# Kernel tuning notes

Measured on AMD Instinct MI355X. Metric: run time of the kernel, lower is better.

## Reference

```python
import jax, jax.numpy as jnp
import numpy as np

N, E, T, IN, H, OUT = 100000, 800000, 8, 3, 32, 64


def _lstm_dir(pre, Whh, bhh, reverse):
    # pre: [T, E, 4H] precomputed input contribution (x @ W_ih^T + b_ih)
    Hh = Whh.shape[1]

    def step(carry, xt):
        h, c = carry
        g = xt + h @ Whh.T + bhh  # [E, 4H], pytorch gate order i,f,g,o
        i = jax.nn.sigmoid(g[:, :Hh])
        f = jax.nn.sigmoid(g[:, Hh:2 * Hh])
        gg = jnp.tanh(g[:, 2 * Hh:3 * Hh])
        o = jax.nn.sigmoid(g[:, 3 * Hh:])
        c = f * c + i * gg
        h = o * jnp.tanh(c)
        return (h, c), None

    init = (jnp.zeros((pre.shape[1], Hh), pre.dtype),
            jnp.zeros((pre.shape[1], Hh), pre.dtype))
    (h, c), _ = jax.lax.scan(step, init, pre, reverse=reverse)
    return c  # final cell state [E, H]


def _mlp(x, W1, W2):
    # MLP(num_layers=2, bias=False): lin1 -> relu -> lin2
    return jax.nn.relu(x @ W1.T) @ W2.T


def setup_inputs() -> dict:
    key = jax.random.key(0)
    ks = jax.random.split(key, 18)
    s = 0.1
    inp = {
        "x": jax.random.normal(ks[0], (N, IN), jnp.float32),
        "edge_traj": jax.random.normal(ks[1], (E, T, 6), jnp.float32),
        "w_ih_f": jax.random.normal(ks[2], (4 * H, 6), jnp.float32) * s,
        "w_hh_f": jax.random.normal(ks[3], (4 * H, H), jnp.float32) * s,
        "b_ih_f": jax.random.normal(ks[4], (4 * H,), jnp.float32) * s,
        "b_hh_f": jax.random.normal(ks[5], (4 * H,), jnp.float32) * s,
        "w_ih_b": jax.random.normal(ks[6], (4 * H, 6), jnp.float32) * s,
        "w_hh_b": jax.random.normal(ks[7], (4 * H, H), jnp.float32) * s,
        "b_ih_b": jax.random.normal(ks[8], (4 * H,), jnp.float32) * s,
        "b_hh_b": jax.random.normal(ks[9], (4 * H,), jnp.float32) * s,
        "coor_w1": jax.random.normal(ks[10], (H, IN), jnp.float32) * s,
        "coor_w2": jax.random.normal(ks[11], (H, H), jnp.float32) * s,
        "nn2_w1": jax.random.normal(ks[12], (H, 3 * H), jnp.float32) * s,
        "nn2_w2": jax.random.normal(ks[13], (H, H), jnp.float32) * s,
        "nn_w1": jax.random.normal(ks[14], (H, H), jnp.float32) * s,
        "nn_w2": jax.random.normal(ks[15], (OUT, H), jnp.float32) * s,
        "edge_index": jax.random.randint(ks[16], (2, E), 0, N, dtype=jnp.int32),
    }
    return inp


def reference(x, edge_traj, w_ih_f, w_hh_f, b_ih_f, b_hh_f,
              w_ih_b, w_hh_b, b_ih_b, b_hh_b,
              coor_w1, coor_w2, nn2_w1, nn2_w2, nn_w1, nn_w2, edge_index):
    # bidirectional 1-layer LSTM over edge trajectories; edge attr = c_t.mean(dim=0)
    pre_f = jnp.einsum('etf,gf->teg', edge_traj, w_ih_f) + b_ih_f
    pre_b = jnp.einsum('etf,gf->teg', edge_traj, w_ih_b) + b_ih_b
    c_f = _lstm_dir(pre_f, w_hh_f, b_hh_f, reverse=False)
    c_b = _lstm_dir(pre_b, w_hh_b, b_hh_b, reverse=True)
    traj_encoding = 0.5 * (c_f + c_b)  # [E, H]

    coor = _mlp(x, coor_w1, coor_w2)  # [N, H]

    src, dst = edge_index[0], edge_index[1]  # flow: source_to_target
    # message: nn2(cat[x_i, x_j, edge_attr]) per edge
    msg_in = jnp.concatenate([coor[dst], coor[src], traj_encoding], axis=-1)  # [E, 3H]
    msg = _mlp(msg_in, nn2_w1, nn2_w2)  # [E, H]
    agg = jax.ops.segment_sum(msg, dst, num_segments=N)  # [N, H]

    out = _mlp(agg, nn_w1, nn_w2)  # [N, OUT]; (note: GINEConv.forward skips (1+eps)*x)
    return out.sum(axis=0)  # [OUT]
```

## Files before the change

### kernel.cpp

```cpp
#include <hip/hip_runtime.h>
#include <hip/hip_bf16.h>

typedef __attribute__((ext_vector_type(8))) short    bf16x8;
typedef __attribute__((ext_vector_type(4))) float    f32x4;
typedef __attribute__((ext_vector_type(4))) unsigned u32x4;

#define MTPW 4
#define LOG2E  1.442695041f
#define LOG2E2 2.885390082f
#define MFMA __builtin_amdgcn_mfma_f32_16x16x32_bf16

__device__ __forceinline__ float rcp_(float v){ return __builtin_amdgcn_rcpf(v); }
__device__ __forceinline__ float exp2_(float v){ return __builtin_amdgcn_exp2f(v); }
__device__ __forceinline__ unsigned pk2(float lo, float hi){
    __hip_bfloat162 h = __float22bfloat162_rn(float2{lo, hi});
    return *(unsigned*)&h;
}
__device__ __forceinline__ float lo2f(unsigned u){ return __uint_as_float(u << 16); }
__device__ __forceinline__ float hi2f(unsigned u){ return __uint_as_float(u & 0xFFFF0000u); }

union U4 { bf16x8 v; unsigned u[4]; };

__device__ __forceinline__ bf16x8 ldw8(const float* __restrict__ p){
    const float4 a = *(const float4*)p;
    const float4 b = *(const float4*)(p + 4);
    U4 r;
    r.u[0] = pk2(a.x, a.y); r.u[1] = pk2(a.z, a.w);
    r.u[2] = pk2(b.x, b.y); r.u[3] = pk2(b.z, b.w);
    return r.v;
}
__device__ __forceinline__ bf16x8 ldw8p(const float* __restrict__ rowp, int lq, float s){
    const float4 a = *(const float4*)(rowp + 4*lq);
    const float4 b = *(const float4*)(rowp + 16 + 4*lq);
    U4 r;
    r.u[0] = pk2(a.x*s, a.y*s); r.u[1] = pk2(a.z*s, a.w*s);
    r.u[2] = pk2(b.x*s, b.y*s); r.u[3] = pk2(b.z*s, b.w*s);
    return r.v;
}

#define LDS_RD8(d0,d1,d2,d3,d4,d5,d6,d7,O0,O1,O2,O3,O4,O5,O6,O7)            \
  asm volatile("ds_read_b128 %0, %8 offset:" O0 "\n\t"                      \
               "ds_read_b128 %1, %8 offset:" O1 "\n\t"                      \
               "ds_read_b128 %2, %8 offset:" O2 "\n\t"                      \
               "ds_read_b128 %3, %8 offset:" O3 "\n\t"                      \
               "ds_read_b128 %4, %8 offset:" O4 "\n\t"                      \
               "ds_read_b128 %5, %8 offset:" O5 "\n\t"                      \
               "ds_read_b128 %6, %8 offset:" O6 "\n\t"                      \
               "ds_read_b128 %7, %8 offset:" O7 "\n\t"                      \
               "s_waitcnt lgkmcnt(0)"                                       \
               : "=&v"(d0),"=&v"(d1),"=&v"(d2),"=&v"(d3),                   \
                 "=&v"(d4),"=&v"(d5),"=&v"(d6),"=&v"(d7)                    \
               : "v"(lds_addr))

__device__ __forceinline__ bf16x8 bc8(u32x4 x){ return __builtin_bit_cast(bf16x8, x); }

__device__ __forceinline__ void gates4_first(const f32x4 ai, const f32x4 ag, const f32x4 ao,
                                             float c[4], float h[4]){
#pragma unroll
    for (int r = 0; r < 4; ++r) {
        const float Ea = exp2_(ai[r]);
        const float Eg = exp2_(ag[r]);
        const float Eo = exp2_(ao[r]);
        c[r] = (Eg - 1.f) * rcp_((Ea + 1.f) * (Eg + 1.f));
        const float Ec = exp2_(LOG2E2 * c[r]);
        h[r] = (Ec - 1.f) * rcp_((Eo + 1.f) * (Ec + 1.f));
    }
}
__device__ __forceinline__ void gates4_mid(const f32x4 ai, const f32x4 af,
                                           const f32x4 ag, const f32x4 ao,
                                           float c[4], float h[4]){
#pragma unroll
    for (int r = 0; r < 4; ++r) {
        const float Ea = exp2_(ai[r]);
        const float Ef = exp2_(af[r]);
        const float Eg = exp2_(ag[r]);
        const float Eo = exp2_(ao[r]);
        const float p  = (Ea + 1.f) * (Eg + 1.f);
        const float f1 = Ef + 1.f;
        const float num = fmaf(c[r], p, (Eg - 1.f) * f1);
        c[r] = num * rcp_(p * f1);
        const float Ec = exp2_(LOG2E2 * c[r]);
        h[r] = (Ec - 1.f) * rcp_((Eo + 1.f) * (Ec + 1.f));
    }
}
__device__ __forceinline__ void gates4_last(const f32x4 ai, const f32x4 af,
                                            const f32x4 ag, float c[4]){
#pragma unroll
    for (int r = 0; r < 4; ++r) {
        const float Ea = exp2_(ai[r]);
        const float Ef = exp2_(af[r]);
        const float Eg = exp2_(ag[r]);
        const float p  = (Ea + 1.f) * (Eg + 1.f);
        const float f1 = Ef + 1.f;
        const float num = fmaf(c[r], p, (Eg - 1.f) * f1);
        c[r] = num * rcp_(p * f1);
    }
}

__global__ __launch_bounds__(256) void coor_kernel(
    const float* __restrict__ x, const float* __restrict__ w1,
    const float* __restrict__ w2, unsigned short* __restrict__ coorb, int N)
{
    __shared__ float sW1[96];
    __shared__ float sW2[1024];
    const int tid = threadIdx.x;
    if (tid < 96) sW1[tid] = w1[tid];
    for (int i = tid; i < 1024; i += 256) sW2[i] = w2[i];
    __syncthreads();
    int n = blockIdx.x * 256 + tid;
    if (n >= N) return;
    const float x0 = x[n*3+0], x1 = x[n*3+1], x2 = x[n*3+2];
    float h[32];
#pragma unroll
    for (int k = 0; k < 32; ++k)
        h[k] = fmaxf(sW1[k*3+0]*x0 + sW1[k*3+1]*x1 + sW1[k*3+2]*x2, 0.0f);
    union { uint4 q[4]; unsigned u[16]; } st;
#pragma unroll
    for (int p = 0; p < 16; ++p) {
        float a0 = 0.f, a1 = 0.f;
#pragma unroll
        for (int k = 0; k < 32; ++k) {
            a0 += sW2[(2*p)  *32 + k] * h[k];
            a1 += sW2[(2*p+1)*32 + k] * h[k];
        }
        st.u[p] = pk2(a0, a1);
    }
    uint4* cp = (uint4*)(coorb + (size_t)n * 32);
#pragma unroll
    for (int w = 0; w < 4; ++w) cp[w] = st.q[w];
}

template<int DIR>
__global__ __launch_bounds__(256, 4) void lstm_kernel(
    const float* __restrict__ edge_traj,
    const float* __restrict__ w_ih, const float* __restrict__ w_hh,
    const float* __restrict__ b_ih, const float* __restrict__ b_hh,
    unsigned* __restrict__ cbuf, int E)
{
    __shared__ unsigned lds_w[4096];
    const int tid = threadIdx.x;
    for (int i = tid; i < 512; i += 256) {
        const int m = i >> 6, ln = i & 63;
        const int le2 = ln & 15, lq2 = ln >> 4;
        const int row = 16*m + le2;
        const float s = (m == 4 || m == 5) ? LOG2E2 : -LOG2E;
        const float4 a = *(const float4*)(w_hh + row*32 + 4*lq2);
        const float4 b = *(const float4*)(w_hh + row*32 + 16 + 4*lq2);
        unsigned* wp = &lds_w[(size_t)i * 4];
        wp[0] = pk2(a.x*s, a.y*s); wp[1] = pk2(a.z*s, a.w*s);
        wp[2] = pk2(b.x*s, b.y*s); wp[3] = pk2(b.z*s, b.w*s);
        unsigned* xp = &lds_w[(size_t)(512 + i) * 4];
        if (lq2 == 0) {
            const float* p = w_ih + row * 6;
            xp[0] = pk2(p[0]*s, p[1]*s);
            xp[1] = pk2(p[2]*s, p[3]*s);
            xp[2] = pk2(p[4]*s, p[5]*s);
            xp[3] = pk2((b_ih[row] + b_hh[row])*s, 0.f);
        } else {
            xp[0] = 0u; xp[1] = 0u; xp[2] = 0u; xp[3] = 0u;
        }
    }
    __syncthreads();

    const int lane = tid & 63;
    const int wid  = tid >> 6;
    const int le   = lane & 15;
    const int lq   = lane >> 4;
    const bool l0  = (lq == 0);
    const unsigned lds_addr = (unsigned)(size_t)lds_w + (unsigned)lane * 16u;
    const f32x4 Z4 = {0.f, 0.f, 0.f, 0.f};

    const long tile = (long)blockIdx.x * 4 + wid;
    const long e0 = tile * 16;
    if (e0 >= E) return;
    const long er = e0 + le;
    const bool valid = er < E;
    const float* xb = edge_traj + (valid ? er : (E - 1)) * 48;

    U4 hf; hf.u[0]=hf.u[1]=hf.u[2]=hf.u[3]=0u;
    float cl[4]={0,0,0,0}, ch[4]={0,0,0,0};

#pragma unroll
    for (int t = 0; t < 8; ++t) {
        const int te = DIR ? (7 - t) : t;
        U4 xf;
        {
            const float* xp = xb + te * 6;
            const float2 a  = *(const float2*)xp;
            const float2 b2 = *(const float2*)(xp + 2);
            const float2 c2 = *(const float2*)(xp + 4);
            xf.u[0] = l0 ? pk2(a.x, a.y)   : 0u;
            xf.u[1] = l0 ? pk2(b2.x, b2.y) : 0u;
            xf.u[2] = l0 ? pk2(c2.x, c2.y) : 0u;
            xf.u[3] = l0 ? 0x3f80u         : 0u;
        }

        u32x4 f0,f1,f2,f3,f4,f5,f6,f7;
        LDS_RD8(f0,f1,f2,f3,f4,f5,f6,f7,
                "0","2048","4096","6144","8192","10240","12288","14336");
        f32x4 ai = MFMA(bc8(f4), xf.v, Z4, 0,0,0);
        f32x4 af = Z4, ao = Z4;
        if (t != 0) af = MFMA(bc8(f5), xf.v, Z4, 0,0,0);
        f32x4 ag = MFMA(bc8(f6), xf.v, Z4, 0,0,0);
        if (t != 7) ao = MFMA(bc8(f7), xf.v, Z4, 0,0,0);
        if (t > 0) {
            ai = MFMA(bc8(f0), hf.v, ai, 0,0,0);
            af = MFMA(bc8(f1), hf.v, af, 0,0,0);
            ag = MFMA(bc8(f2), hf.v, ag, 0,0,0);
            if (t != 7) ao = MFMA(bc8(f3), hf.v, ao, 0,0,0);
        }
        u32x4 g0,g1,g2,g3,g4,g5,g6,g7;
        LDS_RD8(g0,g1,g2,g3,g4,g5,g6,g7,
                "1024","3072","5120","7168","9216","11264","13312","15360");

        float hl[4], hh[4];
        if (t == 0)      gates4_first(ai, ag, ao, cl, hl);
        else if (t == 7) gates4_last(ai, af, ag, cl);
        else             gates4_mid(ai, af, ag, ao, cl, hl);

        f32x4 bi = MFMA(bc8(g4), xf.v, Z4, 0,0,0);
        f32x4 bf = Z4, bo = Z4;
        if (t != 0) bf = MFMA(bc8(g5), xf.v, Z4, 0,0,0);
        f32x4 bg = MFMA(bc8(g6), xf.v, Z4, 0,0,0);
        if (t != 7) bo = MFMA(bc8(g7), xf.v, Z4, 0,0,0);
        if (t > 0) {
            bi = MFMA(bc8(g0), hf.v, bi, 0,0,0);
            bf = MFMA(bc8(g1), hf.v, bf, 0,0,0);
            bg = MFMA(bc8(g2), hf.v, bg, 0,0,0);
            if (t != 7) bo = MFMA(bc8(g3), hf.v, bo, 0,0,0);
        }
        if (t == 0)      gates4_first(bi, bg, bo, ch, hh);
        else if (t == 7) gates4_last(bi, bf, bg, ch);
        else             gates4_mid(bi, bf, bg, bo, ch, hh);

        if (t < 7) {
            hf.u[0] = pk2(hl[0], hl[1]); hf.u[1] = pk2(hl[2], hl[3]);
            hf.u[2] = pk2(hh[0], hh[1]); hf.u[3] = pk2(hh[2], hh[3]);
        }
    }

    if (valid) {
        U4 cw;
        cw.u[0] = pk2(cl[0], cl[1]);
        cw.u[1] = pk2(cl[2], cl[3]);
        cw.u[2] = pk2(ch[0], ch[1]);
        cw.u[3] = pk2(ch[2], ch[3]);
        unsigned* dp = cbuf + er * 16 + lq * 4;
        if (DIR == 0) {
            *(uint4*)dp = *(uint4*)cw.u;
        } else {
            const uint4 f = *(const uint4*)dp;
            uint4 o;
            o.x = pk2(0.5f*(lo2f(f.x)+lo2f(cw.u[0])), 0.5f*(hi2f(f.x)+hi2f(cw.u[0])));
            o.y = pk2(0.5f*(lo2f(f.y)+lo2f(cw.u[1])), 0.5f*(hi2f(f.y)+hi2f(cw.u[1])));
            o.z = pk2(0.5f*(lo2f(f.z)+lo2f(cw.u[2])), 0.5f*(hi2f(f.z)+hi2f(cw.u[2])));
            o.w = pk2(0.5f*(lo2f(f.w)+lo2f(cw.u[3])), 0.5f*(hi2f(f.w)+hi2f(cw.u[3])));
            *(uint4*)dp = o;
        }
    }
}

__global__ __launch_bounds__(256, 4) void msg_kernel(
    unsigned* trmsg,
    const float* __restrict__ nn2_w1, const float* __restrict__ nn2_w2,
    const int* __restrict__ edge_index,
    const unsigned short* __restrict__ coorb, int E)
{
    const int lane = threadIdx.x & 63;
    const int wid  = threadIdx.x >> 6;
    const int le   = lane & 15;
    const int lq   = lane >> 4;
    const f32x4 Z4 = {0.f, 0.f, 0.f, 0.f};

    bf16x8 w1a[2][3], w2a[2];
#pragma unroll
    for (int mm = 0; mm < 2; ++mm) {
        const int row = 16*mm + le;
        w1a[mm][0] = ldw8(nn2_w1 + row*96 +  8*lq);
        w1a[mm][1] = ldw8(nn2_w1 + row*96 + 32 + 8*lq);
        w1a[mm][2] = ldw8p(nn2_w1 + row*96 + 64, lq, 1.0f);
        w2a[mm]    = ldw8p(nn2_w2 + row*32, lq, 1.0f);
    }

    const long gw = (long)blockIdx.x * 4 + wid;
    for (int it = 0; it < MTPW; ++it) {
        const long tile = gw * MTPW + it;
        const long e0 = tile * 16;
        if (e0 >= E) break;
        const long e_raw = e0 + le;
        const bool valid = e_raw < E;
        const long ec = valid ? e_raw : (E - 1);

        U4 tf;
        if (valid) *(uint4*)tf.u = *(const uint4*)(trmsg + e_raw * 16 + lq * 4);
        else tf.u[0] = tf.u[1] = tf.u[2] = tf.u[3] = 0u;

        const int src = edge_index[ec];
        const int dst = edge_index[E + ec];
        U4 df, sf;
        {
            const uint4 dv = *(const uint4*)(coorb + (size_t)dst*32 + lq*8);
            const uint4 sv = *(const uint4*)(coorb + (size_t)src*32 + lq*8);
            df.u[0]=dv.x; df.u[1]=dv.y; df.u[2]=dv.z; df.u[3]=dv.w;
            sf.u[0]=sv.x; sf.u[1]=sv.y; sf.u[2]=sv.z; sf.u[3]=sv.w;
        }

        f32x4 h1[2];
#pragma unroll
        for (int mm = 0; mm < 2; ++mm) {
            f32x4 a = MFMA(w1a[mm][0], df.v, Z4, 0,0,0);
            a = MFMA(w1a[mm][1], sf.v, a, 0,0,0);
            a = MFMA(w1a[mm][2], tf.v, a, 0,0,0);
            h1[mm] = a;
        }
        U4 gf;
        gf.u[0] = pk2(fmaxf(h1[0][0],0.f), fmaxf(h1[0][1],0.f));
        gf.u[1] = pk2(fmaxf(h1[0][2],0.f), fmaxf(h1[0][3],0.f));
        gf.u[2] = pk2(fmaxf(h1[1][0],0.f), fmaxf(h1[1][1],0.f));
        gf.u[3] = pk2(fmaxf(h1[1][2],0.f), fmaxf(h1[1][3],0.f));

        const f32x4 o0 = MFMA(w2a[0], gf.v, Z4, 0,0,0);
        const f32x4 o1 = MFMA(w2a[1], gf.v, Z4, 0,0,0);
        if (valid) {
            U4 cw;
            cw.u[0] = pk2(o0[0], o0[1]);
            cw.u[1] = pk2(o0[2], o0[3]);
            cw.u[2] = pk2(o1[0], o1[1]);
            cw.u[3] = pk2(o1[2], o1[3]);
            *(uint4*)(trmsg + e_raw * 16 + lq * 4) = *(uint4*)cw.u;
        }
    }
}

__global__ __launch_bounds__(256) void hist_kernel(
    const int* __restrict__ ei, int* __restrict__ cnt, int E)
{
    const int e = blockIdx.x*256 + threadIdx.x;
    if (e < E) atomicAdd(&cnt[ei[E + e]], 1);
}

__global__ __launch_bounds__(256) void scan1_kernel(
    const int* __restrict__ cnt, int* __restrict__ bsum, int N)
{
    __shared__ int sp[4];
    const int tid = threadIdx.x;
    const int n = blockIdx.x*256 + tid;
    int c = (n < N) ? cnt[n] : 0;
#pragma unroll
    for (int m = 1; m < 64; m <<= 1) c += __shfl_xor(c, m, 64);
    if ((tid & 63) == 0) sp[tid >> 6] = c;
    __syncthreads();
    if (tid == 0) bsum[blockIdx.x] = sp[0] + sp[1] + sp[2] + sp[3];
}

__global__ __launch_bounds__(512) void scan2_kernel(
    int* __restrict__ bsum, int* __restrict__ offs, int nblk, int E, int N)
{
    __shared__ int s[512];
    const int tid = threadIdx.x;
    const int v = (tid < nblk) ? bsum[tid] : 0;
    s[tid] = v;
    __syncthreads();
    for (int off = 1; off < 512; off <<= 1) {
        const int t = (tid >= off) ? s[tid - off] : 0;
        __syncthreads();
        s[tid] += t;
        __syncthreads();
    }
    if (tid < nblk) bsum[tid] = s[tid] - v;
    if (tid == 0) offs[N] = E;
}

__global__ __launch_bounds__(256) void scan3_kernel(
    const int* __restrict__ cnt, const int* __restrict__ bsum,
    int* __restrict__ offs, int* __restrict__ cursor, int N)
{
    __shared__ int s[256];
    const int tid = threadIdx.x;
    const int n = blockIdx.x*256 + tid;
    const int v = (n < N) ? cnt[n] : 0;
    s[tid] = v;
    __syncthreads();
    for (int off = 1; off < 256; off <<= 1) {
        const int t = (tid >= off) ? s[tid - off] : 0;
        __syncthreads();
        s[tid] += t;
        __syncthreads();
    }
    if (n < N) {
        const int o = bsum[blockIdx.x] + s[tid] - v;
        offs[n] = o;
        cursor[n] = o;
    }
}

__global__ __launch_bounds__(256) void fill_kernel(
    const int* __restrict__ ei, int* __restrict__ cursor,
    int* __restrict__ eidx, int E)
{
    const int e = blockIdx.x*256 + threadIdx.x;
    if (e < E) {
        const int p = atomicAdd(&cursor[ei[E + e]], 1);
        eidx[p] = e;
    }
}

__global__ __launch_bounds__(256) void gather_kernel(
    const unsigned* __restrict__ msg, const int* __restrict__ offs,
    const int* __restrict__ eidx, float* __restrict__ aggv, int N)
{
    const int lane = threadIdx.x & 63;
    const int wid  = threadIdx.x >> 6;
    const int g  = lane >> 4;
    const int le = lane & 15;
    const int n = blockIdx.x*16 + wid*4 + g;
    if (n >= N) return;
    const int beg = offs[n], end = offs[n+1];
    float sx = 0.f, sy = 0.f;
    for (int i = beg; i < end; ++i) {
        const unsigned w = msg[(size_t)eidx[i]*16 + le];
        sx += lo2f(w); sy += hi2f(w);
    }
    *(float2*)(aggv + (size_t)n*32 + 2*le) = float2{sx, sy};
}

__global__ __launch_bounds__(256) void agg_kernel(
    const float* __restrict__ aggv, const float* __restrict__ nn_w1,
    float* __restrict__ partials, int N)
{
    __shared__ float sW[1024];
    __shared__ float sP[4][32];
    const int tid = threadIdx.x;
    for (int i = tid; i < 1024; i += 256) {
        const int jj = i >> 5, s = i & 31, q = s >> 3, j = s & 7;
        const int col = (j < 4) ? (4*q + j) : (16 + 4*q + (j - 4));
        sW[i] = nn_w1[jj*32 + col];
    }
    __syncthreads();
    const int n = blockIdx.x*256 + tid;
    float h[32];
    if (n < N) {
        float a[32];
        const float4* ap = (const float4*)(aggv + (size_t)n*32);
#pragma unroll
        for (int k4 = 0; k4 < 8; ++k4) {
            const float4 v = ap[k4];
            a[k4*4]=v.x; a[k4*4+1]=v.y; a[k4*4+2]=v.z; a[k4*4+3]=v.w;
        }
#pragma unroll
        for (int jj = 0; jj < 32; ++jj) {
            float acc = 0.f;
#pragma unroll
            for (int k = 0; k < 32; ++k) acc += sW[jj*32+k]*a[k];
            h[jj] = fmaxf(acc, 0.f);
        }
    } else {
#pragma unroll
        for (int jj = 0; jj < 32; ++jj) h[jj] = 0.f;
    }
#pragma unroll
    for (int m = 1; m < 64; m <<= 1) {
#pragma unroll
        for (int k = 0; k < 32; ++k) h[k] += __shfl_xor(h[k], m, 64);
    }
    if ((tid & 63) == 0) {
#pragma unroll
        for (int k = 0; k < 32; ++k) sP[tid >> 6][k] = h[k];
    }
    __syncthreads();
    if (tid < 32)
        partials[(size_t)blockIdx.x * 32 + tid]
            = sP[0][tid] + sP[1][tid] + sP[2][tid] + sP[3][tid];
}

__global__ __launch_bounds__(256) void reduce_kernel(
    const float* __restrict__ partials, const float* __restrict__ nn_w2,
    float* __restrict__ out, int nblk)
{
    __shared__ float sR[8][32];
    __shared__ float sS[32];
    const int tid = threadIdx.x;
    const int col = tid & 31;
    const int row = tid >> 5;
    float s = 0.f;
    for (int i = row; i < nblk; i += 8) s += partials[(size_t)i*32 + col];
    sR[row][col] = s;
    __syncthreads();
    if (row == 0) {
        float t = 0.f;
#pragma unroll
        for (int r = 0; r < 8; ++r) t += sR[r][col];
        sS[col] = t;
    }
    __syncthreads();
    if (tid < 64) {
        float acc = 0.f;
#pragma unroll
        for (int k = 0; k < 32; ++k) acc += nn_w2[tid*32+k] * sS[k];
        out[tid] = acc;
    }
}

extern "C" void kernel_launch(void* const* d_in, const int* in_sizes, int n_in,
                              void* d_out, int out_size, void* d_ws, size_t ws_size,
                              hipStream_t stream)
{
    const float* x         = (const float*)d_in[0];
    const float* edge_traj = (const float*)d_in[1];
    const float* w_ih_f    = (const float*)d_in[2];
    const float* w_hh_f    = (const float*)d_in[3];
    const float* b_ih_f    = (const float*)d_in[4];
    const float* b_hh_f    = (const float*)d_in[5];
    const float* w_ih_b    = (const float*)d_in[6];
    const float* w_hh_b    = (const float*)d_in[7];
    const float* b_ih_b    = (const float*)d_in[8];
    const float* b_hh_b    = (const float*)d_in[9];
    const float* coor_w1   = (const float*)d_in[10];
    const float* coor_w2   = (const float*)d_in[11];
    const float* nn2_w1    = (const float*)d_in[12];
    const float* nn2_w2    = (const float*)d_in[13];
    const float* nn_w1     = (const float*)d_in[14];
    const float* nn_w2     = (const float*)d_in[15];
    const int* edge_index  = (const int*)d_in[16];
    const int N = in_sizes[0] / 3;
    const int E = in_sizes[16] / 2;
    const int nblk = (N + 255) / 256;

    float* aggv = (float*)d_ws;
    float* partials = aggv + (size_t)N * 32;
    unsigned short* coorb = (unsigned short*)(partials + (size_t)nblk * 32);
    unsigned* cbuf = (unsigned*)(coorb + (size_t)N * 32);
    int* cnt    = (int*)(cbuf + (size_t)E * 16);
    int* offs   = cnt + N;
    int* cursor = offs + N + 1;
    int* eidx   = cursor + N;
    int* bsum   = eidx + E;

    (void)hipMemsetAsync(cnt, 0, (size_t)N * sizeof(int), stream);

    coor_kernel<<<nblk, 256, 0, stream>>>(x, coor_w1, coor_w2, coorb, N);

    const long tiles   = ((long)E + 15) / 16;
    const int  lblocks = (int)((tiles + 3) / 4);
    lstm_kernel<0><<<lblocks, 256, 0, stream>>>(edge_traj,
        w_ih_f, w_hh_f, b_ih_f, b_hh_f, cbuf, E);
    lstm_kernel<1><<<lblocks, 256, 0, stream>>>(edge_traj,
        w_ih_b, w_hh_b, b_ih_b, b_hh_b, cbuf, E);

    const int eblk = (E + 255) / 256;
    hist_kernel<<<eblk, 256, 0, stream>>>(edge_index, cnt, E);
    scan1_kernel<<<nblk, 256, 0, stream>>>(cnt, bsum, N);
    scan2_kernel<<<1, 512, 0, stream>>>(bsum, offs, nblk, E, N);
    scan3_kernel<<<nblk, 256, 0, stream>>>(cnt, bsum, offs, cursor, N);
    fill_kernel<<<eblk, 256, 0, stream>>>(edge_index, cursor, eidx, E);

    const int mblocks = (int)((tiles + 4*MTPW - 1) / (4*MTPW));
    msg_kernel<<<mblocks, 256, 0, stream>>>(cbuf, nn2_w1, nn2_w2,
        edge_index, coorb, E);

    gather_kernel<<<(N + 15)/16, 256, 0, stream>>>(cbuf, offs, eidx, aggv, N);
    agg_kernel<<<nblk, 256, 0, stream>>>(aggv, nn_w1, partials, N);
    reduce_kernel<<<1, 256, 0, stream>>>(partials, nn_w2, (float*)d_out, nblk);
}
```

Before: 607.0 us.

## Fuse forward and backward LSTM directions into one interleaved kernel

Merges the two per-direction LSTM launches into a single kernel that keeps both directions' weights in LDS and runs the forward and backward recurrences interleaved per timestep. This removes one launch, the second pass over edge_traj, and the read-modify-write of the cell buffer. Interleaving two independent dependency chains is meant to hide MFMA and transcendental latency. In exchange it doubles LDS use to 32 KB per block and raises register pressure, which could lower occupancy under the 4-block launch bound.

```diff
diff --git a/kernel.cpp b/kernel.cpp
--- a/kernel.cpp
+++ b/kernel.cpp
@@ -38,7 +38,7 @@
     return r.v;
 }
 
-#define LDS_RD8(d0,d1,d2,d3,d4,d5,d6,d7,O0,O1,O2,O3,O4,O5,O6,O7)            \
+#define LDS_RD8(AD,d0,d1,d2,d3,d4,d5,d6,d7,O0,O1,O2,O3,O4,O5,O6,O7)         \
   asm volatile("ds_read_b128 %0, %8 offset:" O0 "\n\t"                      \
                "ds_read_b128 %1, %8 offset:" O1 "\n\t"                      \
                "ds_read_b128 %2, %8 offset:" O2 "\n\t"                      \
@@ -50,9 +50,21 @@
                "s_waitcnt lgkmcnt(0)"                                       \
                : "=&v"(d0),"=&v"(d1),"=&v"(d2),"=&v"(d3),                   \
                  "=&v"(d4),"=&v"(d5),"=&v"(d6),"=&v"(d7)                    \
-               : "v"(lds_addr))
+               : "v"(AD))
 
 __device__ __forceinline__ bf16x8 bc8(u32x4 x){ return __builtin_bit_cast(bf16x8, x); }
+
+#define GRP(AI,AF,AG,AO, Q0,Q1,Q2,Q3,Q4,Q5,Q6,Q7, XF, HF)                   \
+    AI = MFMA(bc8(Q4), XF.v, Z4, 0,0,0);                                    \
+    AF = (t != 0) ? MFMA(bc8(Q5), XF.v, Z4, 0,0,0) : Z4;                    \
+    AG = MFMA(bc8(Q6), XF.v, Z4, 0,0,0);                                    \
+    AO = (t != 7) ? MFMA(bc8(Q7), XF.v, Z4, 0,0,0) : Z4;                    \
+    if (t > 0) {                                                            \
+        AI = MFMA(bc8(Q0), HF.v, AI, 0,0,0);                                \
+        AF = MFMA(bc8(Q1), HF.v, AF, 0,0,0);                                \
+        AG = MFMA(bc8(Q2), HF.v, AG, 0,0,0);                                \
+        if (t != 7) AO = MFMA(bc8(Q3), HF.v, AO, 0,0,0);                    \
+    }
 
 __device__ __forceinline__ void gates4_first(const f32x4 ai, const f32x4 ag, const f32x4 ao,
                                              float c[4], float h[4]){
@@ -96,6 +108,10 @@
         c[r] = num * rcp_(p * f1);
     }
 }
+#define GATES(AI,AF,AG,AO,C,H)                                              \
+    if (t == 0)      gates4_first(AI, AG, AO, C, H);                        \
+    else if (t == 7) gates4_last(AI, AF, AG, C);                            \
+    else             gates4_mid(AI, AF, AG, AO, C, H);
 
 __global__ __launch_bounds__(256) void coor_kernel(
     const float* __restrict__ x, const float* __restrict__ w1,
@@ -130,32 +146,39 @@
     for (int w = 0; w < 4; ++w) cp[w] = st.q[w];
 }
 
-template<int DIR>
 __global__ __launch_bounds__(256, 4) void lstm_kernel(
     const float* __restrict__ edge_traj,
-    const float* __restrict__ w_ih, const float* __restrict__ w_hh,
-    const float* __restrict__ b_ih, const float* __restrict__ b_hh,
+    const float* __restrict__ w_ih_f, const float* __restrict__ w_hh_f,
+    const float* __restrict__ b_ih_f, const float* __restrict__ b_hh_f,
+    const float* __restrict__ w_ih_b, const float* __restrict__ w_hh_b,
+    const float* __restrict__ b_ih_b, const float* __restrict__ b_hh_b,
     unsigned* __restrict__ cbuf, int E)
 {
-    __shared__ unsigned lds_w[4096];
-    const int tid = threadIdx.x;
-    for (int i = tid; i < 512; i += 256) {
-        const int m = i >> 6, ln = i & 63;
+    __shared__ unsigned lds_w[8192];
+    const int tid = threadIdx.x;
+    for (int i = tid; i < 1024; i += 256) {
+        const int dir = i >> 9;
+        const int idx = i & 511;
+        const int m = idx >> 6, ln = idx & 63;
         const int le2 = ln & 15, lq2 = ln >> 4;
         const int row = 16*m + le2;
         const float s = (m == 4 || m == 5) ? LOG2E2 : -LOG2E;
-        const float4 a = *(const float4*)(w_hh + row*32 + 4*lq2);
-        const float4 b = *(const float4*)(w_hh + row*32 + 16 + 4*lq2);
-        unsigned* wp = &lds_w[(size_t)i * 4];
+        const float* whh = dir ? w_hh_b : w_hh_f;
+        const float* wih = dir ? w_ih_b : w_ih_f;
+        const float* bi  = dir ? b_ih_b : b_ih_f;
+        const float* bh  = dir ? b_hh_b : b_hh_f;
+        const float4 a = *(const float4*)(whh + row*32 + 4*lq2);
+        const float4 b = *(const float4*)(whh + row*32 + 16 + 4*lq2);
+        unsigned* wp = &lds_w[(size_t)dir*4096 + (size_t)idx*4];
         wp[0] = pk2(a.x*s, a.y*s); wp[1] = pk2(a.z*s, a.w*s);
         wp[2] = pk2(b.x*s, b.y*s); wp[3] = pk2(b.z*s, b.w*s);
-        unsigned* xp = &lds_w[(size_t)(512 + i) * 4];
+        unsigned* xp = &lds_w[(size_t)dir*4096 + 2048 + (size_t)idx*4];
         if (lq2 == 0) {
-            const float* p = w_ih + row * 6;
+            const float* p = wih + row * 6;
             xp[0] = pk2(p[0]*s, p[1]*s);
             xp[1] = pk2(p[2]*s, p[3]*s);
             xp[2] = pk2(p[4]*s, p[5]*s);
-            xp[3] = pk2((b_ih[row] + b_hh[row])*s, 0.f);
+            xp[3] = pk2((bi[row] + bh[row])*s, 0.f);
         } else {
             xp[0] = 0u; xp[1] = 0u; xp[2] = 0u; xp[3] = 0u;
         }
@@ -167,7 +190,8 @@
     const int le   = lane & 15;
     const int lq   = lane >> 4;
     const bool l0  = (lq == 0);
-    const unsigned lds_addr = (unsigned)(size_t)lds_w + (unsigned)lane * 16u;
+    const unsigned adF = (unsigned)(size_t)lds_w + (unsigned)lane * 16u;
+    const unsigned adB = adF + 16384u;
     const f32x4 Z4 = {0.f, 0.f, 0.f, 0.f};
 
     const long tile = (long)blockIdx.x * 4 + wid;
@@ -177,86 +201,79 @@
     const bool valid = er < E;
     const float* xb = edge_traj + (valid ? er : (E - 1)) * 48;
 
-    U4 hf; hf.u[0]=hf.u[1]=hf.u[2]=hf.u[3]=0u;
-    float cl[4]={0,0,0,0}, ch[4]={0,0,0,0};
+    U4 hfF, hfB;
+    hfF.u[0]=hfF.u[1]=hfF.u[2]=hfF.u[3]=0u;
+    hfB.u[0]=hfB.u[1]=hfB.u[2]=hfB.u[3]=0u;
+    float clF[4]={0,0,0,0}, chF[4]={0,0,0,0};
+    float clB[4]={0,0,0,0}, chB[4]={0,0,0,0};
 
 #pragma unroll
     for (int t = 0; t < 8; ++t) {
-        const int te = DIR ? (7 - t) : t;
-        U4 xf;
+        U4 xfF, xfB;
         {
-            const float* xp = xb + te * 6;
+            const float* xp = xb + t * 6;
             const float2 a  = *(const float2*)xp;
             const float2 b2 = *(const float2*)(xp + 2);
             const float2 c2 = *(const float2*)(xp + 4);
-            xf.u[0] = l0 ? pk2(a.x, a.y)   : 0u;
-            xf.u[1] = l0 ? pk2(b2.x, b2.y) : 0u;
-            xf.u[2] = l0 ? pk2(c2.x, c2.y) : 0u;
-            xf.u[3] = l0 ? 0x3f80u         : 0u;
-        }
-
-        u32x4 f0,f1,f2,f3,f4,f5,f6,f7;
-        LDS_RD8(f0,f1,f2,f3,f4,f5,f6,f7,
+            xfF.u[0] = l0 ? pk2(a.x, a.y)   : 0u;
+            xfF.u[1] = l0 ? pk2(b2.x, b2.y) : 0u;
+            xfF.u[2] = l0 ? pk2(c2.x, c2.y) : 0u;
+            xfF.u[3] = l0 ? 0x3f80u         : 0u;
+        }
+        {
+            const float* xp = xb + (7 - t) * 6;
+            const float2 a  = *(const float2*)xp;
+            const float2 b2 = *(const float2*)(xp + 2);
+            const float2 c2 = *(const float2*)(xp + 4);
+            xfB.u[0] = l0 ? pk2(a.x, a.y)   : 0u;
+            xfB.u[1] = l0 ? pk2(b2.x, b2.y) : 0u;
+            xfB.u[2] = l0 ? pk2(c2.x, c2.y) : 0u;
+            xfB.u[3] = l0 ? 0x3f80u         : 0u;
+        }
+
+        u32x4 a0,a1,a2,a3,a4,a5,a6,a7;
+        LDS_RD8(adF, a0,a1,a2,a3,a4,a5,a6,a7,
                 "0","2048","4096","6144","8192","10240","12288","14336");
-        f32x4 ai = MFMA(bc8(f4), xf.v, Z4, 0,0,0);
-        f32x4 af = Z4, ao = Z4;
-        if (t != 0) af = MFMA(bc8(f5), xf.v, Z4, 0,0,0);
-        f32x4 ag = MFMA(bc8(f6), xf.v, Z4, 0,0,0);
-        if (t != 7) ao = MFMA(bc8(f7), xf.v, Z4, 0,0,0);
-        if (t > 0) {
-            ai = MFMA(bc8(f0), hf.v, ai, 0,0,0);
-            af = MFMA(bc8(f1), hf.v, af, 0,0,0);
-            ag = MFMA(bc8(f2), hf.v, ag, 0,0,0);
-            if (t != 7) ao = MFMA(bc8(f3), hf.v, ao, 0,0,0);
-        }
-        u32x4 g0,g1,g2,g3,g4,g5,g6,g7;
-        LDS_RD8(g0,g1,g2,g3,g4,g5,g6,g7,
+        f32x4 fiL,ffL,fgL,foL;
+        GRP(fiL,ffL,fgL,foL, a0,a1,a2,a3,a4,a5,a6,a7, xfF, hfF);
+        u32x4 b0,b1,b2,b3,b4,b5,b6,b7;
+        LDS_RD8(adB, b0,b1,b2,b3,b4,b5,b6,b7,
+                "0","2048","4096","6144","8192","10240","12288","14336");
+        f32x4 biL,bfL,bgL,boL;
+        GRP(biL,bfL,bgL,boL, b0,b1,b2,b3,b4,b5,b6,b7, xfB, hfB);
+        float hlF[4], hlB[4];
+        GATES(fiL,ffL,fgL,foL, clF, hlF);
+        GATES(biL,bfL,bgL,boL, clB, hlB);
+
+        u32x4 c0,c1,c2,c3,c4,c5,c6,c7;
+        LDS_RD8(adF, c0,c1,c2,c3,c4,c5,c6,c7,
                 "1024","3072","5120","7168","9216","11264","13312","15360");
-
-        float hl[4], hh[4];
-        if (t == 0)      gates4_first(ai, ag, ao, cl, hl);
-        else if (t == 7) gates4_last(ai, af, ag, cl);
-        else             gates4_mid(ai, af, ag, ao, cl, hl);
-
-        f32x4 bi = MFMA(bc8(g4), xf.v, Z4, 0,0,0);
-        f32x4 bf = Z4, bo = Z4;
-        if (t != 0) bf = MFMA(bc8(g5), xf.v, Z4, 0,0,0);
-        f32x4 bg = MFMA(bc8(g6), xf.v, Z4, 0,0,0);
-        if (t != 7) bo = MFMA(bc8(g7), xf.v, Z4, 0,0,0);
-        if (t > 0) {
-            bi = MFMA(bc8(g0), hf.v, bi, 0,0,0);
-            bf = MFMA(bc8(g1), hf.v, bf, 0,0,0);
-            bg = MFMA(bc8(g2), hf.v, bg, 0,0,0);
-            if (t != 7) bo = MFMA(bc8(g3), hf.v, bo, 0,0,0);
-        }
-        if (t == 0)      gates4_first(bi, bg, bo, ch, hh);
-        else if (t == 7) gates4_last(bi, bf, bg, ch);
-        else             gates4_mid(bi, bf, bg, bo, ch, hh);
+        f32x4 fiH,ffH,fgH,foH;
+        GRP(fiH,ffH,fgH,foH, c0,c1,c2,c3,c4,c5,c6,c7, xfF, hfF);
+        u32x4 d0,d1,d2,d3,d4,d5,d6,d7;
+        LDS_RD8(adB, d0,d1,d2,d3,d4,d5,d6,d7,
+                "1024","3072","5120","7168","9216","11264","13312","15360");
+        f32x4 biH,bfH,bgH,boH;
+        GRP(biH,bfH,bgH,boH, d0,d1,d2,d3,d4,d5,d6,d7, xfB, hfB);
+        float hhF[4], hhB[4];
+        GATES(fiH,ffH,fgH,foH, chF, hhF);
+        GATES(biH,bfH,bgH,boH, chB, hhB);
 
         if (t < 7) {
-            hf.u[0] = pk2(hl[0], hl[1]); hf.u[1] = pk2(hl[2], hl[3]);
-            hf.u[2] = pk2(hh[0], hh[1]); hf.u[3] = pk2(hh[2], hh[3]);
+            hfF.u[0] = pk2(hlF[0], hlF[1]); hfF.u[1] = pk2(hlF[2], hlF[3]);
+            hfF.u[2] = pk2(hhF[0], hhF[1]); hfF.u[3] = pk2(hhF[2], hhF[3]);
+            hfB.u[0] = pk2(hlB[0], hlB[1]); hfB.u[1] = pk2(hlB[2], hlB[3]);
+            hfB.u[2] = pk2(hhB[0], hhB[1]); hfB.u[3] = pk2(hhB[2], hhB[3]);
         }
     }
 
     if (valid) {
         U4 cw;
-        cw.u[0] = pk2(cl[0], cl[1]);
-        cw.u[1] = pk2(cl[2], cl[3]);
-        cw.u[2] = pk2(ch[0], ch[1]);
-        cw.u[3] = pk2(ch[2], ch[3]);
-        unsigned* dp = cbuf + er * 16 + lq * 4;
-        if (DIR == 0) {
-            *(uint4*)dp = *(uint4*)cw.u;
-        } else {
-            const uint4 f = *(const uint4*)dp;
-            uint4 o;
-            o.x = pk2(0.5f*(lo2f(f.x)+lo2f(cw.u[0])), 0.5f*(hi2f(f.x)+hi2f(cw.u[0])));
-            o.y = pk2(0.5f*(lo2f(f.y)+lo2f(cw.u[1])), 0.5f*(hi2f(f.y)+hi2f(cw.u[1])));
-            o.z = pk2(0.5f*(lo2f(f.z)+lo2f(cw.u[2])), 0.5f*(hi2f(f.z)+hi2f(cw.u[2])));
-            o.w = pk2(0.5f*(lo2f(f.w)+lo2f(cw.u[3])), 0.5f*(hi2f(f.w)+hi2f(cw.u[3])));
-            *(uint4*)dp = o;
-        }
+        cw.u[0] = pk2(0.5f*(clF[0]+clB[0]), 0.5f*(clF[1]+clB[1]));
+        cw.u[1] = pk2(0.5f*(clF[2]+clB[2]), 0.5f*(clF[3]+clB[3]));
+        cw.u[2] = pk2(0.5f*(chF[0]+chB[0]), 0.5f*(chF[1]+chB[1]));
+        cw.u[3] = pk2(0.5f*(chF[2]+chB[2]), 0.5f*(chF[3]+chB[3]));
+        *(uint4*)(cbuf + er * 16 + lq * 4) = *(uint4*)cw.u;
     }
 }
 
@@ -542,9 +559,8 @@
 
     const long tiles   = ((long)E + 15) / 16;
     const int  lblocks = (int)((tiles + 3) / 4);
-    lstm_kernel<0><<<lblocks, 256, 0, stream>>>(edge_traj,
-        w_ih_f, w_hh_f, b_ih_f, b_hh_f, cbuf, E);
-    lstm_kernel<1><<<lblocks, 256, 0, stream>>>(edge_traj,
+    lstm_kernel<<<lblocks, 256, 0, stream>>>(edge_traj,
+        w_ih_f, w_hh_f, b_ih_f, b_hh_f,
         w_ih_b, w_hh_b, b_ih_b, b_hh_b, cbuf, E);
 
     const int eblk = (E + 255) / 256;
```

Result: no change. 608.3 us (+0.2%).

## Fuse edge message MLP into backward LSTM kernel and preload trajectory inputs

Applied to the files above, without the earlier changes.

The separate message kernel is removed, and its work (gathering the coor features and running the two-layer MLP over the concatenated input) is folded into the epilogue of the backward-direction LSTM kernel. The averaged cell state now stays in registers instead of being written and then re-read. All eight timestep inputs are loaded up front before the recurrence. This cuts one kernel launch and one full read/write pass over the edge buffer. In exchange, the LSTM kernel uses more registers, which may lower occupancy, and each wave reloads the MLP weights instead of amortising them over several tiles.

```diff
diff --git a/kernel.cpp b/kernel.cpp
--- a/kernel.cpp
+++ b/kernel.cpp
@@ -5,7 +5,6 @@
 typedef __attribute__((ext_vector_type(4))) float    f32x4;
 typedef __attribute__((ext_vector_type(4))) unsigned u32x4;
 
-#define MTPW 4
 #define LOG2E  1.442695041f
 #define LOG2E2 2.885390082f
 #define MFMA __builtin_amdgcn_mfma_f32_16x16x32_bf16
@@ -29,16 +28,16 @@
     r.u[2] = pk2(b.x, b.y); r.u[3] = pk2(b.z, b.w);
     return r.v;
 }
-__device__ __forceinline__ bf16x8 ldw8p(const float* __restrict__ rowp, int lq, float s){
+__device__ __forceinline__ bf16x8 ldw8p(const float* __restrict__ rowp, int lq){
     const float4 a = *(const float4*)(rowp + 4*lq);
     const float4 b = *(const float4*)(rowp + 16 + 4*lq);
     U4 r;
-    r.u[0] = pk2(a.x*s, a.y*s); r.u[1] = pk2(a.z*s, a.w*s);
-    r.u[2] = pk2(b.x*s, b.y*s); r.u[3] = pk2(b.z*s, b.w*s);
+    r.u[0] = pk2(a.x, a.y); r.u[1] = pk2(a.z, a.w);
+    r.u[2] = pk2(b.x, b.y); r.u[3] = pk2(b.z, b.w);
     return r.v;
 }
 
-#define LDS_RD8(d0,d1,d2,d3,d4,d5,d6,d7,O0,O1,O2,O3,O4,O5,O6,O7)            \
+#define LDS_RD8(AD,d0,d1,d2,d3,d4,d5,d6,d7,O0,O1,O2,O3,O4,O5,O6,O7)         \
   asm volatile("ds_read_b128 %0, %8 offset:" O0 "\n\t"                      \
                "ds_read_b128 %1, %8 offset:" O1 "\n\t"                      \
                "ds_read_b128 %2, %8 offset:" O2 "\n\t"                      \
@@ -50,7 +49,7 @@
                "s_waitcnt lgkmcnt(0)"                                       \
                : "=&v"(d0),"=&v"(d1),"=&v"(d2),"=&v"(d3),                   \
                  "=&v"(d4),"=&v"(d5),"=&v"(d6),"=&v"(d7)                    \
-               : "v"(lds_addr))
+               : "v"(AD))
 
 __device__ __forceinline__ bf16x8 bc8(u32x4 x){ return __builtin_bit_cast(bf16x8, x); }
 
@@ -135,7 +134,10 @@
     const float* __restrict__ edge_traj,
     const float* __restrict__ w_ih, const float* __restrict__ w_hh,
     const float* __restrict__ b_ih, const float* __restrict__ b_hh,
-    unsigned* __restrict__ cbuf, int E)
+    unsigned* __restrict__ cbuf,
+    const float* __restrict__ nn2_w1, const float* __restrict__ nn2_w2,
+    const int* __restrict__ edge_index,
+    const unsigned short* __restrict__ coorb, int E)
 {
     __shared__ unsigned lds_w[4096];
     const int tid = threadIdx.x;
@@ -175,34 +177,36 @@
     if (e0 >= E) return;
     const long er = e0 + le;
     const bool valid = er < E;
-    const float* xb = edge_traj + (valid ? er : (E - 1)) * 48;
+    const long ec = valid ? er : (E - 1);
+    const float* xb = edge_traj + ec * 48;
+
+    U4 xf[8];
+#pragma unroll
+    for (int t = 0; t < 8; ++t) {
+        const int te = DIR ? (7 - t) : t;
+        const float* xp = xb + te * 6;
+        const float2 a  = *(const float2*)xp;
+        const float2 b2 = *(const float2*)(xp + 2);
+        const float2 c2 = *(const float2*)(xp + 4);
+        xf[t].u[0] = l0 ? pk2(a.x, a.y)   : 0u;
+        xf[t].u[1] = l0 ? pk2(b2.x, b2.y) : 0u;
+        xf[t].u[2] = l0 ? pk2(c2.x, c2.y) : 0u;
+        xf[t].u[3] = l0 ? 0x3f80u         : 0u;
+    }
 
     U4 hf; hf.u[0]=hf.u[1]=hf.u[2]=hf.u[3]=0u;
     float cl[4]={0,0,0,0}, ch[4]={0,0,0,0};
 
 #pragma unroll
     for (int t = 0; t < 8; ++t) {
-        const int te = DIR ? (7 - t) : t;
-        U4 xf;
-        {
-            const float* xp = xb + te * 6;
-            const float2 a  = *(const float2*)xp;
-            const float2 b2 = *(const float2*)(xp + 2);
-            const float2 c2 = *(const float2*)(xp + 4);
-            xf.u[0] = l0 ? pk2(a.x, a.y)   : 0u;
-            xf.u[1] = l0 ? pk2(b2.x, b2.y) : 0u;
-            xf.u[2] = l0 ? pk2(c2.x, c2.y) : 0u;
-            xf.u[3] = l0 ? 0x3f80u         : 0u;
-        }
-
         u32x4 f0,f1,f2,f3,f4,f5,f6,f7;
-        LDS_RD8(f0,f1,f2,f3,f4,f5,f6,f7,
+        LDS_RD8(lds_addr, f0,f1,f2,f3,f4,f5,f6,f7,
                 "0","2048","4096","6144","8192","10240","12288","14336");
-        f32x4 ai = MFMA(bc8(f4), xf.v, Z4, 0,0,0);
+        f32x4 ai = MFMA(bc8(f4), xf[t].v, Z4, 0,0,0);
         f32x4 af = Z4, ao = Z4;
-        if (t != 0) af = MFMA(bc8(f5), xf.v, Z4, 0,0,0);
-        f32x4 ag = MFMA(bc8(f6), xf.v, Z4, 0,0,0);
-        if (t != 7) ao = MFMA(bc8(f7), xf.v, Z4, 0,0,0);
+        if (t != 0) af = MFMA(bc8(f5), xf[t].v, Z4, 0,0,0);
+        f32x4 ag = MFMA(bc8(f6), xf[t].v, Z4, 0,0,0);
+        if (t != 7) ao = MFMA(bc8(f7), xf[t].v, Z4, 0,0,0);
         if (t > 0) {
             ai = MFMA(bc8(f0), hf.v, ai, 0,0,0);
             af = MFMA(bc8(f1), hf.v, af, 0,0,0);
@@ -210,7 +214,7 @@
             if (t != 7) ao = MFMA(bc8(f3), hf.v, ao, 0,0,0);
         }
         u32x4 g0,g1,g2,g3,g4,g5,g6,g7;
-        LDS_RD8(g0,g1,g2,g3,g4,g5,g6,g7,
+        LDS_RD8(lds_addr, g0,g1,g2,g3,g4,g5,g6,g7,
                 "1024","3072","5120","7168","9216","11264","13312","15360");
 
         float hl[4], hh[4];
@@ -218,11 +222,11 @@
         else if (t == 7) gates4_last(ai, af, ag, cl);
         else             gates4_mid(ai, af, ag, ao, cl, hl);
 
-        f32x4 bi = MFMA(bc8(g4), xf.v, Z4, 0,0,0);
+        f32x4 bi = MFMA(bc8(g4), xf[t].v, Z4, 0,0,0);
         f32x4 bf = Z4, bo = Z4;
-        if (t != 0) bf = MFMA(bc8(g5), xf.v, Z4, 0,0,0);
-        f32x4 bg = MFMA(bc8(g6), xf.v, Z4, 0,0,0);
-        if (t != 7) bo = MFMA(bc8(g7), xf.v, Z4, 0,0,0);
+        if (t != 0) bf = MFMA(bc8(g5), xf[t].v, Z4, 0,0,0);
+        f32x4 bg = MFMA(bc8(g6), xf[t].v, Z4, 0,0,0);
+        if (t != 7) bo = MFMA(bc8(g7), xf[t].v, Z4, 0,0,0);
         if (t > 0) {
             bi = MFMA(bc8(g0), hf.v, bi, 0,0,0);
             bf = MFMA(bc8(g1), hf.v, bf, 0,0,0);
@@ -239,61 +243,32 @@
         }
     }
 
-    if (valid) {
-        U4 cw;
-        cw.u[0] = pk2(cl[0], cl[1]);
-        cw.u[1] = pk2(cl[2], cl[3]);
-        cw.u[2] = pk2(ch[0], ch[1]);
-        cw.u[3] = pk2(ch[2], ch[3]);
-        unsigned* dp = cbuf + er * 16 + lq * 4;
-        if (DIR == 0) {
-            *(uint4*)dp = *(uint4*)cw.u;
-        } else {
-            const uint4 f = *(const uint4*)dp;
-            uint4 o;
-            o.x = pk2(0.5f*(lo2f(f.x)+lo2f(cw.u[0])), 0.5f*(hi2f(f.x)+hi2f(cw.u[0])));
-            o.y = pk2(0.5f*(lo2f(f.y)+lo2f(cw.u[1])), 0.5f*(hi2f(f.y)+hi2f(cw.u[1])));
-            o.z = pk2(0.5f*(lo2f(f.z)+lo2f(cw.u[2])), 0.5f*(hi2f(f.z)+hi2f(cw.u[2])));
-            o.w = pk2(0.5f*(lo2f(f.w)+lo2f(cw.u[3])), 0.5f*(hi2f(f.w)+hi2f(cw.u[3])));
-            *(uint4*)dp = o;
-        }
-    }
-}
-
-__global__ __launch_bounds__(256, 4) void msg_kernel(
-    unsigned* trmsg,
-    const float* __restrict__ nn2_w1, const float* __restrict__ nn2_w2,
-    const int* __restrict__ edge_index,
-    const unsigned short* __restrict__ coorb, int E)
-{
-    const int lane = threadIdx.x & 63;
-    const int wid  = threadIdx.x >> 6;
-    const int le   = lane & 15;
-    const int lq   = lane >> 4;
-    const f32x4 Z4 = {0.f, 0.f, 0.f, 0.f};
-
-    bf16x8 w1a[2][3], w2a[2];
-#pragma unroll
-    for (int mm = 0; mm < 2; ++mm) {
-        const int row = 16*mm + le;
-        w1a[mm][0] = ldw8(nn2_w1 + row*96 +  8*lq);
-        w1a[mm][1] = ldw8(nn2_w1 + row*96 + 32 + 8*lq);
-        w1a[mm][2] = ldw8p(nn2_w1 + row*96 + 64, lq, 1.0f);
-        w2a[mm]    = ldw8p(nn2_w2 + row*32, lq, 1.0f);
-    }
-
-    const long gw = (long)blockIdx.x * 4 + wid;
-    for (int it = 0; it < MTPW; ++it) {
-        const long tile = gw * MTPW + it;
-        const long e0 = tile * 16;
-        if (e0 >= E) break;
-        const long e_raw = e0 + le;
-        const bool valid = e_raw < E;
-        const long ec = valid ? e_raw : (E - 1);
-
-        U4 tf;
-        if (valid) *(uint4*)tf.u = *(const uint4*)(trmsg + e_raw * 16 + lq * 4);
-        else tf.u[0] = tf.u[1] = tf.u[2] = tf.u[3] = 0u;
+    if (DIR == 0) {
+        if (valid) {
+            U4 cw;
+            cw.u[0] = pk2(cl[0], cl[1]);
+            cw.u[1] = pk2(cl[2], cl[3]);
+            cw.u[2] = pk2(ch[0], ch[1]);
+            cw.u[3] = pk2(ch[2], ch[3]);
+            *(uint4*)(cbuf + er * 16 + lq * 4) = *(uint4*)cw.u;
+        }
+    } else {
+        const uint4 f = *(const uint4*)(cbuf + ec * 16 + lq * 4);
+        U4 trf;
+        trf.u[0] = pk2(0.5f*(lo2f(f.x)+cl[0]), 0.5f*(hi2f(f.x)+cl[1]));
+        trf.u[1] = pk2(0.5f*(lo2f(f.y)+cl[2]), 0.5f*(hi2f(f.y)+cl[3]));
+        trf.u[2] = pk2(0.5f*(lo2f(f.z)+ch[0]), 0.5f*(hi2f(f.z)+ch[1]));
+        trf.u[3] = pk2(0.5f*(lo2f(f.w)+ch[2]), 0.5f*(hi2f(f.w)+ch[3]));
+
+        bf16x8 w1a[2][3], w2a[2];
+#pragma unroll
+        for (int mm = 0; mm < 2; ++mm) {
+            const int row = 16*mm + le;
+            w1a[mm][0] = ldw8(nn2_w1 + row*96 +  8*lq);
+            w1a[mm][1] = ldw8(nn2_w1 + row*96 + 32 + 8*lq);
+            w1a[mm][2] = ldw8p(nn2_w1 + row*96 + 64, lq);
+            w2a[mm]    = ldw8p(nn2_w2 + row*32, lq);
+        }
 
         const int src = edge_index[ec];
         const int dst = edge_index[E + ec];
@@ -310,7 +285,7 @@
         for (int mm = 0; mm < 2; ++mm) {
             f32x4 a = MFMA(w1a[mm][0], df.v, Z4, 0,0,0);
             a = MFMA(w1a[mm][1], sf.v, a, 0,0,0);
-            a = MFMA(w1a[mm][2], tf.v, a, 0,0,0);
+            a = MFMA(w1a[mm][2], trf.v, a, 0,0,0);
             h1[mm] = a;
         }
         U4 gf;
@@ -327,7 +302,7 @@
             cw.u[1] = pk2(o0[2], o0[3]);
             cw.u[2] = pk2(o1[0], o1[1]);
             cw.u[3] = pk2(o1[2], o1[3]);
-            *(uint4*)(trmsg + e_raw * 16 + lq * 4) = *(uint4*)cw.u;
+            *(uint4*)(cbuf + er * 16 + lq * 4) = *(uint4*)cw.u;
         }
     }
 }
@@ -543,9 +518,8 @@
     const long tiles   = ((long)E + 15) / 16;
     const int  lblocks = (int)((tiles + 3) / 4);
     lstm_kernel<0><<<lblocks, 256, 0, stream>>>(edge_traj,
-        w_ih_f, w_hh_f, b_ih_f, b_hh_f, cbuf, E);
-    lstm_kernel<1><<<lblocks, 256, 0, stream>>>(edge_traj,
-        w_ih_b, w_hh_b, b_ih_b, b_hh_b, cbuf, E);
+        w_ih_f, w_hh_f, b_ih_f, b_hh_f, cbuf,
+        nn2_w1, nn2_w2, edge_index, coorb, E);
 
     const int eblk = (E + 255) / 256;
     hist_kernel<<<eblk, 256, 0, stream>>>(edge_index, cnt, E);
@@ -554,9 +528,9 @@
     scan3_kernel<<<nblk, 256, 0, stream>>>(cnt, bsum, offs, cursor, N);
     fill_kernel<<<eblk, 256, 0, stream>>>(edge_index, cursor, eidx, E);
 
-    const int mblocks = (int)((tiles + 4*MTPW - 1) / (4*MTPW));
-    msg_kernel<<<mblocks, 256, 0, stream>>>(cbuf, nn2_w1, nn2_w2,
-        edge_index, coorb, E);
+    lstm_kernel<1><<<lblocks, 256, 0, stream>>>(edge_traj,
+        w_ih_b, w_hh_b, b_ih_b, b_hh_b, cbuf,
+        nn2_w1, nn2_w2, edge_index, coorb, E);
 
     gather_kernel<<<(N + 15)/16, 256, 0, stream>>>(cbuf, offs, eidx, aggv, N);
     agg_kernel<<<nblk, 256, 0, stream>>>(aggv, nn_w1, partials, N);
```

Measured after the change: 626.3 us. 1.03x slower.
